# Performance work log

Measured on AMD Instinct MI355X. Metric: run time of the kernel, lower is better.

## Reference

```python
import jax, jax.numpy as jnp
import numpy as np

VOCAB, X_SIZE, H_SIZE, N_CLASSES = 50000, 300, 150, 5
DEPTH = 18                      # complete binary tree, N = 2^(DEPTH+1)-1 nodes
N_NODES = 2 ** (DEPTH + 1) - 1  # 524287
SCALE = 0.05                    # param init scale for numerical sanity


def setup_inputs() -> dict:
    key = jax.random.key(0)
    ks = jax.random.split(key, 8)
    return {
        "x_id": jax.random.randint(ks[0], (N_NODES,), 0, VOCAB, dtype=jnp.int32),
        "emb": jax.random.normal(ks[1], (VOCAB, X_SIZE), jnp.float32) * SCALE,
        "W_iou": jax.random.normal(ks[2], (X_SIZE, 3 * H_SIZE), jnp.float32) * SCALE,
        "U_iou": jax.random.normal(ks[3], (H_SIZE, 3 * H_SIZE), jnp.float32) * SCALE,
        "b_iou": jnp.zeros((3 * H_SIZE,), jnp.float32),
        "W_f": jax.random.normal(ks[4], (X_SIZE, H_SIZE), jnp.float32) * SCALE,
        "U_f": jax.random.normal(ks[5], (H_SIZE, H_SIZE), jnp.float32) * SCALE,
        "b_f": jnp.zeros((H_SIZE,), jnp.float32),
        "W_out": jax.random.normal(ks[6], (H_SIZE, N_CLASSES), jnp.float32) * SCALE,
        "b_out": jnp.zeros((N_CLASSES,), jnp.float32),
    }


def reference(x_id, emb, W_iou, U_iou, b_iou, W_f, U_f, b_f, W_out, b_out):
    # Child-Sum TreeLSTM propagated leaves->root over a complete binary tree
    # stored in heap layout: children of node i are 2i+1, 2i+2.
    N = x_id.shape[0]
    H = U_iou.shape[0]
    depth = int(np.log2(N + 1)) - 1

    x = emb[x_id]  # input_module: embedding lookup  [N, X]
    h = jnp.zeros((N, H), x.dtype)
    c = jnp.zeros((N, H), x.dtype)

    # level-batched topological propagation (19 static levels)
    for lvl in range(depth, -1, -1):
        s, e = 2 ** lvl - 1, 2 ** (lvl + 1) - 1  # node range of this level
        xl = x[s:e]                              # [n_l, X]
        if lvl == depth:  # leaves: zero child state
            h_sum = jnp.zeros((e - s, H), x.dtype)
            fc_sum = jnp.zeros((e - s, H), x.dtype)
        else:
            # children of consecutive nodes are contiguous: [2s+1, 2e+1)
            hc = h[2 * s + 1:2 * e + 1].reshape(e - s, 2, H)
            cc = c[2 * s + 1:2 * e + 1].reshape(e - s, 2, H)
            h_sum = hc.sum(axis=1)               # reduce: sum child h
            # per-child forget gate
            f = jax.nn.sigmoid((xl @ W_f)[:, None, :] + hc @ U_f + b_f)
            fc_sum = (f * cc).sum(axis=1)
        iou = xl @ W_iou + h_sum @ U_iou + b_iou  # [n_l, 3H]
        i, o, u = jnp.split(iou, 3, axis=-1)
        c_new = jax.nn.sigmoid(i) * jnp.tanh(u) + fc_sum
        h_new = jax.nn.sigmoid(o) * jnp.tanh(c_new)
        h = h.at[s:e].set(h_new)
        c = c.at[s:e].set(c_new)

    return h @ W_out + b_out  # output_module: Linear(H, C)  [N, C]
```

## Files before the change

### kernel.cpp

```cpp
#include <hip/hip_runtime.h>
#include <cstdint>

typedef _Float16 f16_t;
typedef __attribute__((ext_vector_type(8))) _Float16 f16x8;
typedef __attribute__((ext_vector_type(4))) _Float16 f16x4;
typedef __attribute__((ext_vector_type(4))) float f32x4;

#define HP      160
#define NCOL    640
#define KXP     320
#define NNODES  524287
#define LEAF_S  262143
#define LEAF_M  262144
#define NVOCAB  50000
#define AST     168

__device__ __forceinline__ float frcp(float x) { return __builtin_amdgcn_rcpf(x); }
__device__ __forceinline__ float sigf(float x) { return frcp(1.0f + __expf(-x)); }
__device__ __forceinline__ float tanhf_(float x) {
  return 1.0f - 2.0f * frcp(1.0f + __expf(2.0f * x));
}
__device__ __forceinline__ f16x8 zero8() {
  f16x8 z;
#pragma unroll
  for (int i = 0; i < 8; ++i) z[i] = (_Float16)0.0f;
  return z;
}
__device__ __forceinline__ f32x4 zero4() {
  f32x4 z;
#pragma unroll
  for (int i = 0; i < 4; ++i) z[i] = 0.0f;
  return z;
}

__global__ void prep_params(const float* __restrict__ W_iou, const float* __restrict__ U_iou,
                            const float* __restrict__ b_iou, const float* __restrict__ W_f,
                            const float* __restrict__ U_f, const float* __restrict__ b_f,
                            f16_t* __restrict__ WreT, f16_t* __restrict__ UreT,
                            float* __restrict__ bre) {
  int idx = blockIdx.x * 256 + threadIdx.x;
  if (idx < NCOL * KXP) {
    int col = idx / KXP, k = idx % KXP;
    int j = col >> 2, g = col & 3;
    float v = 0.0f;
    if (k < 300 && j < 150) v = (g < 3) ? W_iou[k * 450 + g * 150 + j] : W_f[k * 150 + j];
    WreT[idx] = (f16_t)v;
  } else if (idx < NCOL * KXP + NCOL * HP) {
    int i2 = idx - NCOL * KXP;
    int col = i2 / HP, k = i2 % HP;
    int g = col / 160, j = col % 160;
    float v = 0.0f;
    if (k < 150 && j < 150) v = (g < 3) ? U_iou[k * 450 + g * 150 + j] : U_f[k * 150 + j];
    UreT[i2] = (f16_t)v;
  } else if (idx < NCOL * KXP + NCOL * HP + NCOL) {
    int col = idx - (NCOL * KXP + NCOL * HP);
    int j = col >> 2, g = col & 3;
    bre[col] = (j < 150) ? ((g < 3) ? b_iou[g * 150 + j] : b_f[j]) : 0.0f;
  }
}

__global__ __launch_bounds__(256) void gemm_p(const float* __restrict__ emb,
                                              const f16_t* __restrict__ WreT,
                                              const float* __restrict__ bre,
                                              f16_t* __restrict__ P) {
  __shared__ __align__(16) f16_t A_sh[64 * 328];
  __shared__ __align__(16) f16_t B_sh[128 * 40];
  const int tid = threadIdx.x;
  const int wid = tid >> 6, lane = tid & 63, l15 = lane & 15, q = lane >> 4;
  const int row0 = blockIdx.x * 64;

#pragma unroll
  for (int i = 0; i < 10; ++i) {
    int ch = tid + 256 * i;
    int r = ch / 40, kc = (ch % 40) * 8;
    int grow = row0 + r;
    f16x8 hv;
    if (grow < NVOCAB && kc + 8 <= 300) {
      float4 a = *(const float4*)&emb[grow * 300 + kc];
      float4 b = *(const float4*)&emb[grow * 300 + kc + 4];
      hv[0] = (_Float16)a.x; hv[1] = (_Float16)a.y; hv[2] = (_Float16)a.z; hv[3] = (_Float16)a.w;
      hv[4] = (_Float16)b.x; hv[5] = (_Float16)b.y; hv[6] = (_Float16)b.z; hv[7] = (_Float16)b.w;
    } else {
#pragma unroll
      for (int e = 0; e < 8; ++e) {
        int k = kc + e;
        float v = (grow < NVOCAB && k < 300) ? emb[grow * 300 + k] : 0.0f;
        hv[e] = (_Float16)v;
      }
    }
    *(f16x8*)&A_sh[r * 328 + kc] = hv;
  }
  __syncthreads();

  for (int bn = 0; bn < 5; ++bn) {
    const int col0 = bn * 128;
    f32x4 acc[8];
#pragma unroll
    for (int t = 0; t < 8; ++t) acc[t] = zero4();
    for (int kk = 0; kk < KXP; kk += 32) {
#pragma unroll
      for (int i = 0; i < 2; ++i) {
        int ch = tid + 256 * i;
        int cidx = ch >> 2, kc = (ch & 3) * 8;
        *(f16x8*)&B_sh[cidx * 40 + kc] =
            *(const f16x8*)&WreT[(col0 + cidx) * KXP + kk + kc];
      }
      __syncthreads();
      f16x8 af = *(const f16x8*)&A_sh[(16 * wid + l15) * 328 + kk + q * 8];
#pragma unroll
      for (int t = 0; t < 8; ++t) {
        f16x8 bfr = *(const f16x8*)&B_sh[(t * 16 + l15) * 40 + q * 8];
        acc[t] = __builtin_amdgcn_mfma_f32_16x16x32_f16(af, bfr, acc[t], 0, 0, 0);
      }
      __syncthreads();
    }
#pragma unroll
    for (int t = 0; t < 8; ++t) {
      int col = col0 + t * 16 + l15;
      float bias = bre[col];
#pragma unroll
      for (int r2 = 0; r2 < 4; ++r2) {
        int row = row0 + 16 * wid + q * 4 + r2;
        if (row < NVOCAB) P[(long)row * NCOL + col] = (f16_t)(acc[t][r2] + bias);
      }
    }
  }
}

__global__ void leafhc_kernel(const f16_t* __restrict__ P, f16_t* __restrict__ Hleaf,
                              f16_t* __restrict__ Cleaf) {
  int idx = blockIdx.x * 256 + threadIdx.x;
  if (idx >= NVOCAB * 80) return;
  int v = idx / 80, t = idx % 80;
  f16x8 pk = *(const f16x8*)&P[(long)v * NCOL + t * 8];
#pragma unroll
  for (int e = 0; e < 2; ++e) {
    float iv = (float)pk[e * 4 + 0], ov = (float)pk[e * 4 + 1], uv = (float)pk[e * 4 + 2];
    float cl = sigf(iv) * tanhf_(uv);
    float hl = sigf(ov) * tanhf_(cl);
    Hleaf[(long)v * HP + t * 2 + e] = (f16_t)hl;
    Cleaf[(long)v * HP + t * 2 + e] = (f16_t)cl;
  }
}

__global__ void oleaf_kernel(const f16_t* __restrict__ Hleaf, const float* __restrict__ W_out,
                             const float* __restrict__ b_out, float* __restrict__ Oleaf) {
  const int tid = threadIdx.x;
  const int row = blockIdx.x * 16 + (tid >> 4), l = tid & 15;
  if (row >= NVOCAB) return;
  float acc[5] = {0, 0, 0, 0, 0};
  for (int j = l; j < 150; j += 16) {
    float hv = (float)Hleaf[(long)row * HP + j];
#pragma unroll
    for (int m = 0; m < 5; ++m) acc[m] += hv * W_out[j * 5 + m];
  }
#pragma unroll
  for (int m = 0; m < 5; ++m) {
    float vv = acc[m];
    vv += __shfl_xor(vv, 1);
    vv += __shfl_xor(vv, 2);
    vv += __shfl_xor(vv, 4);
    vv += __shfl_xor(vv, 8);
    if (l == 0) Oleaf[(long)row * 8 + m] = vv + b_out[m];
  }
}

__global__ void leafout_kernel(const int* __restrict__ x_id, const float* __restrict__ Oleaf,
                               float* __restrict__ out) {
  int leaf = blockIdx.x * 256 + threadIdx.x;
  int xv = x_id[LEAF_S + leaf];
  const float* O = Oleaf + (long)xv * 8;
  float4 o4 = *(const float4*)O;
  float o5 = O[4];
  long base = ((long)LEAF_S + leaf) * 5;
  out[base + 0] = o4.x; out[base + 1] = o4.y; out[base + 2] = o4.z;
  out[base + 3] = o4.w; out[base + 4] = o5;
}

__global__ __launch_bounds__(256, 3) void level17_kernel(
    const int* __restrict__ x_id, const f16_t* __restrict__ P,
    const f16_t* __restrict__ UreT, const f16_t* __restrict__ Hleaf,
    const f16_t* __restrict__ Cleaf, f16_t* __restrict__ Hout,
    f16_t* __restrict__ Cout, const float* __restrict__ W_out,
    const float* __restrict__ b_out, float* __restrict__ out) {
  __shared__ __align__(16) f16_t A_sh[64 * AST];
  __shared__ __align__(16) f16_t B_sh[128 * 40];
  const int tid = threadIdx.x;
  const int wid = tid >> 6, lane = tid & 63, l15 = lane & 15, q = lane >> 4;
  const int p0 = blockIdx.x * 32;
  const int s1 = (1 << 17) - 1;
  const long childbase = 2L * s1 + 1 + 2 * p0;

#pragma unroll
  for (int i = 0; i < 5; ++i) {
    int ch = tid + 256 * i;
    int r = ch / 20, kc = (ch % 20) * 8;
    int xv = x_id[childbase + r];
    *(f16x8*)&A_sh[r * AST + kc] = *(const f16x8*)&Hleaf[(long)xv * HP + kc];
  }
  __syncthreads();

  int xvp[2], xvl[2], xvr[2];
#pragma unroll
  for (int rr = 0; rr < 2; ++rr) {
    int pl = 8 * wid + 2 * q + rr;
    xvp[rr] = x_id[(long)s1 + p0 + pl];
    xvl[rr] = x_id[childbase + 2 * pl];
    xvr[rr] = x_id[childbase + 2 * pl + 1];
  }
  float oacc[2][5] = {};

  for (int jt = 0; jt < 5; ++jt) {
    const int j0 = jt * 32;
    f32x4 acc[4][2];
#pragma unroll
    for (int g = 0; g < 4; ++g)
#pragma unroll
      for (int jh = 0; jh < 2; ++jh) acc[g][jh] = zero4();

    for (int kk = 0; kk < HP; kk += 32) {
#pragma unroll
      for (int i = 0; i < 2; ++i) {
        int ch = tid + 256 * i;
        int cidx = ch >> 2, kc = (ch & 3) * 8;
        int g = cidx >> 5, jj = cidx & 31;
        int col = g * HP + j0 + jj;
        *(f16x8*)&B_sh[cidx * 40 + kc] = *(const f16x8*)&UreT[col * HP + kk + kc];
      }
      __syncthreads();
      f16x8 af = *(const f16x8*)&A_sh[(16 * wid + l15) * AST + kk + q * 8];
#pragma unroll
      for (int g = 0; g < 4; ++g)
#pragma unroll
        for (int jh = 0; jh < 2; ++jh) {
          f16x8 bfr = *(const f16x8*)&B_sh[(g * 32 + jh * 16 + l15) * 40 + q * 8];
          acc[g][jh] = __builtin_amdgcn_mfma_f32_16x16x32_f16(af, bfr, acc[g][jh], 0, 0, 0);
        }
      __syncthreads();
    }

#pragma unroll
    for (int rr = 0; rr < 2; ++rr) {
      const int r = rr * 2;
      const int pl = 8 * wid + 2 * q + rr;
      const f16_t* Prp = P + (long)xvp[rr] * NCOL;
#pragma unroll
      for (int jh = 0; jh < 2; ++jh) {
        const int j = j0 + jh * 16 + l15;
        f16x4 pp = *(const f16x4*)&Prp[j * 4];
        float ipre = (float)pp[0] + acc[0][jh][r] + acc[0][jh][r + 1];
        float opre = (float)pp[1] + acc[1][jh][r] + acc[1][jh][r + 1];
        float upre = (float)pp[2] + acc[2][jh][r] + acc[2][jh][r + 1];
        float pf   = (float)pp[3];
        float fl = sigf(pf + acc[3][jh][r]);
        float fr = sigf(pf + acc[3][jh][r + 1]);
        float clv = (float)Cleaf[(long)xvl[rr] * HP + j];
        float crv = (float)Cleaf[(long)xvr[rr] * HP + j];
        float cn = sigf(ipre) * tanhf_(upre) + fl * clv + fr * crv;
        float hn = sigf(opre) * tanhf_(cn);
        Hout[(long)(p0 + pl) * HP + j] = (f16_t)hn;
        Cout[(long)(p0 + pl) * HP + j] = (f16_t)cn;
        int wbase = (j < 150) ? j * 5 : 0;
#pragma unroll
        for (int m = 0; m < 5; ++m) oacc[rr][m] += hn * W_out[wbase + m];
      }
    }
  }

#pragma unroll
  for (int rr = 0; rr < 2; ++rr) {
    int pl = 8 * wid + 2 * q + rr;
#pragma unroll
    for (int m = 0; m < 5; ++m) {
      float v = oacc[rr][m];
      v += __shfl_xor(v, 1);
      v += __shfl_xor(v, 2);
      v += __shfl_xor(v, 4);
      v += __shfl_xor(v, 8);
      if (l15 == 0) out[((long)s1 + p0 + pl) * 5 + m] = v + b_out[m];
    }
  }
}

template <bool LEAF>
__global__ __launch_bounds__(256, 3) void fused_kernel(
    const int* __restrict__ x_id, const f16_t* __restrict__ P,
    const f16_t* __restrict__ UreT, const f16_t* __restrict__ Hc,
    const f16_t* __restrict__ Cc, f16_t* __restrict__ Hout,
    f16_t* __restrict__ Cout, const float* __restrict__ W_out,
    const float* __restrict__ b_out, float* __restrict__ out, int s1, int M1) {
  __shared__ __align__(16) f16_t A_sh[64 * AST];
  __shared__ __align__(16) f16_t A2_sh[32 * AST];
  __shared__ __align__(16) f16_t B_sh[128 * 40];
  __shared__ f16_t C_sh[32 * 160];
  const int tid = threadIdx.x;
  const int wid = tid >> 6, lane = tid & 63, l15 = lane & 15, q = lane >> 4;
  const int p0 = blockIdx.x * 32;
  const long childbase = 2L * s1 + 1 + 2 * p0;

#pragma unroll
  for (int i = 0; i < 5; ++i) {
    int ch = tid + 256 * i;
    int r = ch / 20, kc = (ch % 20) * 8;
    f16x8 v;
    if (LEAF) {
      int xv = x_id[childbase + r];
      v = *(const f16x8*)&Hc[(long)xv * HP + kc];
    } else {
      v = *(const f16x8*)&Hc[(long)(2 * p0 + r) * HP + kc];
    }
    *(f16x8*)&A_sh[r * AST + kc] = v;
  }
  __syncthreads();

  int xvp[2], xvl[2], xvr[2];
#pragma unroll
  for (int rr = 0; rr < 2; ++rr) {
    int pl = 8 * wid + 2 * q + rr;
    long pn = (long)s1 + p0 + pl;
    xvp[rr] = x_id[pn];
    if (LEAF) {
      xvl[rr] = x_id[childbase + 2 * pl];
      xvr[rr] = x_id[childbase + 2 * pl + 1];
    }
  }
  float oacc1[2][5] = {};

  for (int jt = 0; jt < 5; ++jt) {
    const int j0 = jt * 32;
    f32x4 acc[4][2];
#pragma unroll
    for (int g = 0; g < 4; ++g)
#pragma unroll
      for (int jh = 0; jh < 2; ++jh) acc[g][jh] = zero4();

    for (int kk = 0; kk < HP; kk += 32) {
#pragma unroll
      for (int i = 0; i < 2; ++i) {
        int ch = tid + 256 * i;
        int cidx = ch >> 2, kc = (ch & 3) * 8;
        int g = cidx >> 5, jj = cidx & 31;
        int col = g * HP + j0 + jj;
        *(f16x8*)&B_sh[cidx * 40 + kc] = *(const f16x8*)&UreT[col * HP + kk + kc];
      }
      __syncthreads();
      f16x8 af = *(const f16x8*)&A_sh[(16 * wid + l15) * AST + kk + q * 8];
#pragma unroll
      for (int g = 0; g < 4; ++g)
#pragma unroll
        for (int jh = 0; jh < 2; ++jh) {
          f16x8 bfr = *(const f16x8*)&B_sh[(g * 32 + jh * 16 + l15) * 40 + q * 8];
          acc[g][jh] = __builtin_amdgcn_mfma_f32_16x16x32_f16(af, bfr, acc[g][jh], 0, 0, 0);
        }
      __syncthreads();
    }

#pragma unroll
    for (int rr = 0; rr < 2; ++rr) {
      const int r = rr * 2;
      const int lr0 = 16 * wid + q * 4 + r;
      const int pl = lr0 >> 1;
      const f16_t* Prp = P + (long)xvp[rr] * NCOL;
#pragma unroll
      for (int jh = 0; jh < 2; ++jh) {
        const int j = j0 + jh * 16 + l15;
        f16x4 pp = *(const f16x4*)&Prp[j * 4];
        float ipre = (float)pp[0] + acc[0][jh][r] + acc[0][jh][r + 1];
        float opre = (float)pp[1] + acc[1][jh][r] + acc[1][jh][r + 1];
        float upre = (float)pp[2] + acc[2][jh][r] + acc[2][jh][r + 1];
        float pf   = (float)pp[3];
        float fl = sigf(pf + acc[3][jh][r]);
        float fr = sigf(pf + acc[3][jh][r + 1]);
        float clv, crv;
        if (LEAF) {
          clv = (float)Cc[(long)xvl[rr] * HP + j];
          crv = (float)Cc[(long)xvr[rr] * HP + j];
        } else {
          clv = (float)Cc[(long)(2 * p0 + lr0) * HP + j];
          crv = (float)Cc[(long)(2 * p0 + lr0 + 1) * HP + j];
        }
        float cn = sigf(ipre) * tanhf_(upre) + fl * clv + fr * crv;
        float hn = sigf(opre) * tanhf_(cn);
        A2_sh[pl * AST + j] = (f16_t)hn;
        C_sh[pl * 160 + j] = (f16_t)cn;
        int wbase = (j < 150) ? j * 5 : 0;
#pragma unroll
        for (int m = 0; m < 5; ++m) oacc1[rr][m] += hn * W_out[wbase + m];
      }
    }
  }

#pragma unroll
  for (int rr = 0; rr < 2; ++rr) {
    int pl = 8 * wid + 2 * q + rr;
#pragma unroll
    for (int m = 0; m < 5; ++m) {
      float v = oacc1[rr][m];
      v += __shfl_xor(v, 1);
      v += __shfl_xor(v, 2);
      v += __shfl_xor(v, 4);
      v += __shfl_xor(v, 8);
      if (l15 == 0) out[((long)s1 + p0 + pl) * 5 + m] = v + b_out[m];
    }
  }

  const int s2 = (s1 - 1) >> 1;
  const int p02 = p0 >> 1;
  const bool act2 = (wid < 2);
  int xvp2[2];
#pragma unroll
  for (int rr = 0; rr < 2; ++rr) {
    int pl = 8 * wid + 2 * q + rr;
    long pn = (long)s2 + p02 + (act2 ? pl : 0);
    xvp2[rr] = x_id[pn];
  }
  float oacc2[2][5] = {};

  for (int jt = 0; jt < 5; ++jt) {
    const int j0 = jt * 32;
    f32x4 acc[4][2];
#pragma unroll
    for (int g = 0; g < 4; ++g)
#pragma unroll
      for (int jh = 0; jh < 2; ++jh) acc[g][jh] = zero4();

    for (int kk = 0; kk < HP; kk += 32) {
#pragma unroll
      for (int i = 0; i < 2; ++i) {
        int ch = tid + 256 * i;
        int cidx = ch >> 2, kc = (ch & 3) * 8;
        int g = cidx >> 5, jj = cidx & 31;
        int col = g * HP + j0 + jj;
        *(f16x8*)&B_sh[cidx * 40 + kc] = *(const f16x8*)&UreT[col * HP + kk + kc];
      }
      __syncthreads();
      if (act2) {
        f16x8 af = *(const f16x8*)&A2_sh[(16 * wid + l15) * AST + kk + q * 8];
#pragma unroll
        for (int g = 0; g < 4; ++g)
#pragma unroll
          for (int jh = 0; jh < 2; ++jh) {
            f16x8 bfr = *(const f16x8*)&B_sh[(g * 32 + jh * 16 + l15) * 40 + q * 8];
            acc[g][jh] = __builtin_amdgcn_mfma_f32_16x16x32_f16(af, bfr, acc[g][jh], 0, 0, 0);
          }
      }
      __syncthreads();
    }

    if (act2) {
#pragma unroll
      for (int rr = 0; rr < 2; ++rr) {
        const int r = rr * 2;
        const int lr0 = 16 * wid + q * 4 + r;
        const int pl = lr0 >> 1;
        const f16_t* Prp = P + (long)xvp2[rr] * NCOL;
#pragma unroll
        for (int jh = 0; jh < 2; ++jh) {
          const int j = j0 + jh * 16 + l15;
          f16x4 pp = *(const f16x4*)&Prp[j * 4];
          float ipre = (float)pp[0] + acc[0][jh][r] + acc[0][jh][r + 1];
          float opre = (float)pp[1] + acc[1][jh][r] + acc[1][jh][r + 1];
          float upre = (float)pp[2] + acc[2][jh][r] + acc[2][jh][r + 1];
          float pf   = (float)pp[3];
          float fl = sigf(pf + acc[3][jh][r]);
          float fr = sigf(pf + acc[3][jh][r + 1]);
          float clv = (float)C_sh[lr0 * 160 + j];
          float crv = (float)C_sh[(lr0 + 1) * 160 + j];
          float cn = sigf(ipre) * tanhf_(upre) + fl * clv + fr * crv;
          float hn = sigf(opre) * tanhf_(cn);
          Hout[(long)(p02 + pl) * HP + j] = (f16_t)hn;
          Cout[(long)(p02 + pl) * HP + j] = (f16_t)cn;
          int wbase = (j < 150) ? j * 5 : 0;
#pragma unroll
          for (int m = 0; m < 5; ++m) oacc2[rr][m] += hn * W_out[wbase + m];
        }
      }
    }
  }

  if (act2) {
#pragma unroll
    for (int rr = 0; rr < 2; ++rr) {
      int pl = 8 * wid + 2 * q + rr;
#pragma unroll
      for (int m = 0; m < 5; ++m) {
        float v = oacc2[rr][m];
        v += __shfl_xor(v, 1);
        v += __shfl_xor(v, 2);
        v += __shfl_xor(v, 4);
        v += __shfl_xor(v, 8);
        if (l15 == 0) out[((long)s2 + p02 + pl) * 5 + m] = v + b_out[m];
      }
    }
  }
}

__global__ __launch_bounds__(256) void small_level(
    const int* __restrict__ x_id, const f16_t* __restrict__ P,
    const f16_t* __restrict__ UreT, const f16_t* __restrict__ Hc,
    const f16_t* __restrict__ Cc, f16_t* __restrict__ Hp, f16_t* __restrict__ Cp,
    const float* __restrict__ W_out, const float* __restrict__ b_out,
    float* __restrict__ out, int s) {
  __shared__ __align__(16) f16_t hlr[320];
  __shared__ float partial[4][5];
  const int tid = threadIdx.x;
  const int p = blockIdx.x;
  const long cb = (long)(2 * p) * HP;

  if (tid < 40) *(f16x8*)&hlr[tid * 8] = *(const f16x8*)&Hc[cb + tid * 8];
  __syncthreads();

  const int j = tid;
  float ai = 0.f, ao = 0.f, au = 0.f, afl = 0.f, afr = 0.f;
  float hn = 0.f;
  float contrib[5] = {0.f, 0.f, 0.f, 0.f, 0.f};
  if (j < HP) {
    const f16_t* Ui = &UreT[(long)(0 * HP + j) * HP];
    const f16_t* Uo = &UreT[(long)(1 * HP + j) * HP];
    const f16_t* Uu = &UreT[(long)(2 * HP + j) * HP];
    const f16_t* Uf = &UreT[(long)(3 * HP + j) * HP];
#pragma unroll 5
    for (int k8 = 0; k8 < 19; ++k8) {
      f16x8 hl8 = *(const f16x8*)&hlr[k8 * 8];
      f16x8 hr8 = *(const f16x8*)&hlr[160 + k8 * 8];
      f16x8 ui8 = *(const f16x8*)&Ui[k8 * 8];
      f16x8 uo8 = *(const f16x8*)&Uo[k8 * 8];
      f16x8 uu8 = *(const f16x8*)&Uu[k8 * 8];
      f16x8 uf8 = *(const f16x8*)&Uf[k8 * 8];
#pragma unroll
      for (int e = 0; e < 8; ++e) {
        float hlv = (float)hl8[e], hrv = (float)hr8[e];
        float hsv = hlv + hrv;
        ai  += hsv * (float)ui8[e];
        ao  += hsv * (float)uo8[e];
        au  += hsv * (float)uu8[e];
        afl += hlv * (float)uf8[e];
        afr += hrv * (float)uf8[e];
      }
    }
    int xv = x_id[(long)s + p];
    f16x4 pp = *(const f16x4*)&P[(long)xv * NCOL + j * 4];
    float ipre = (float)pp[0] + ai;
    float opre = (float)pp[1] + ao;
    float upre = (float)pp[2] + au;
    float pf   = (float)pp[3];
    float fl = sigf(pf + afl), fr = sigf(pf + afr);
    float clv = (float)Cc[cb + j];
    float crv = (float)Cc[cb + HP + j];
    float cn = sigf(ipre) * tanhf_(upre) + fl * clv + fr * crv;
    hn = sigf(opre) * tanhf_(cn);
    Hp[(long)p * HP + j] = (f16_t)hn;
    Cp[(long)p * HP + j] = (f16_t)cn;
    int wbase = (j < 150) ? j * 5 : 0;
#pragma unroll
    for (int m = 0; m < 5; ++m) contrib[m] = hn * W_out[wbase + m];
  }
  const int w = tid >> 6, l = tid & 63;
#pragma unroll
  for (int m = 0; m < 5; ++m) {
    float v = contrib[m];
    v += __shfl_xor(v, 1);  v += __shfl_xor(v, 2);  v += __shfl_xor(v, 4);
    v += __shfl_xor(v, 8);  v += __shfl_xor(v, 16); v += __shfl_xor(v, 32);
    if (l == 0) partial[w][m] = v;
  }
  __syncthreads();
  if (tid < 5) {
    float v = partial[0][tid] + partial[1][tid] + partial[2][tid] + partial[3][tid];
    out[((long)s + p) * 5 + tid] = v + b_out[tid];
  }
}

extern "C" void kernel_launch(void* const* d_in, const int* in_sizes, int n_in,
                              void* d_out, int out_size, void* d_ws, size_t ws_size,
                              hipStream_t stream) {
  const int* x_id   = (const int*)d_in[0];
  const float* emb  = (const float*)d_in[1];
  const float* W_iou = (const float*)d_in[2];
  const float* U_iou = (const float*)d_in[3];
  const float* b_iou = (const float*)d_in[4];
  const float* W_f   = (const float*)d_in[5];
  const float* U_f   = (const float*)d_in[6];
  const float* b_f   = (const float*)d_in[7];
  const float* W_out = (const float*)d_in[8];
  const float* b_out = (const float*)d_in[9];
  float* out = (float*)d_out;
  char* ws = (char*)d_ws;

  f16_t* WreT  = (f16_t*)(ws + 0);
  f16_t* UreT  = (f16_t*)(ws + 409600);
  float* bre   = (float*)(ws + 614400);
  f16_t* P     = (f16_t*)(ws + 616960);
  f16_t* Hleaf = (f16_t*)(ws + 64616960);
  f16_t* Cleaf = (f16_t*)(ws + 80616960);
  float* Oleaf = (float*)(ws + 96616960);
  f16_t* H17   = (f16_t*)(ws + 96616960);
  f16_t* C17   = (f16_t*)(ws + 138560000);
  f16_t* H15 = (f16_t*)(ws + 64616960);
  f16_t* C15 = (f16_t*)(ws + 75102720);
  f16_t* H13 = (f16_t*)(ws + 96616960);
  f16_t* C13 = (f16_t*)(ws + 99238400);
  char* vb = ws + 85588480;
  f16_t* VH[13]; f16_t* VC[13];
  for (int L = 12; L >= 0; --L) {
    size_t rows = (size_t)1 << L;
    VH[L] = (f16_t*)vb; vb += rows * 320;
    VC[L] = (f16_t*)vb; vb += rows * 320;
  }

  prep_params<<<1203, 256, 0, stream>>>(W_iou, U_iou, b_iou, W_f, U_f, b_f, WreT, UreT, bre);
  gemm_p<<<782, 256, 0, stream>>>(emb, WreT, bre, P);
  leafhc_kernel<<<15625, 256, 0, stream>>>(P, Hleaf, Cleaf);
  oleaf_kernel<<<3125, 256, 0, stream>>>(Hleaf, W_out, b_out, Oleaf);
  leafout_kernel<<<1024, 256, 0, stream>>>(x_id, Oleaf, out);

  level17_kernel<<<4096, 256, 0, stream>>>(x_id, P, UreT, Hleaf, Cleaf, H17, C17,
                                           W_out, b_out, out);
  fused_kernel<false><<<2048, 256, 0, stream>>>(x_id, P, UreT, H17, C17, H15, C15,
                                                W_out, b_out, out, (1 << 16) - 1, 1 << 16);
  fused_kernel<false><<<512, 256, 0, stream>>>(x_id, P, UreT, H15, C15, H13, C13,
                                               W_out, b_out, out, (1 << 14) - 1, 1 << 14);
  small_level<<<4096, 256, 0, stream>>>(x_id, P, UreT, H13, C13, VH[12], VC[12],
                                        W_out, b_out, out, (1 << 12) - 1);
  for (int L = 11; L >= 0; --L) {
    small_level<<<(1 << L), 256, 0, stream>>>(x_id, P, UreT, VH[L + 1], VC[L + 1],
                                              VH[L], VC[L], W_out, b_out, out,
                                              (1 << L) - 1);
  }

  (void)in_sizes; (void)n_in; (void)out_size; (void)ws_size;
}
```

Baseline: 991.3 us.

## Batch four parents per block in small levels with interleaved U layout

The small_level kernel now processes four parent nodes per block, so each U weight load is reused across four parents instead of one. A new interleaved UP2 weight layout, built in prep_params, packs the i/o/u/f gates for two consecutive k values into one 8-wide f16 vector, giving coalesced loads across j. This cuts U-matrix traffic and block count for the upper levels, but raises register pressure, leaves blocks underfilled at the tiny top levels, and needs bounds guards on the child-row loads.

```diff
diff --git a/kernel.cpp b/kernel.cpp
--- a/kernel.cpp
+++ b/kernel.cpp
@@ -4,6 +4,7 @@
 typedef _Float16 f16_t;
 typedef __attribute__((ext_vector_type(8))) _Float16 f16x8;
 typedef __attribute__((ext_vector_type(4))) _Float16 f16x4;
+typedef __attribute__((ext_vector_type(2))) _Float16 f16x2;
 typedef __attribute__((ext_vector_type(4))) float f32x4;
 
 #define HP      160
@@ -14,6 +15,7 @@
 #define LEAF_M  262144
 #define NVOCAB  50000
 #define AST     168
+#define PPB     4
 
 __device__ __forceinline__ float frcp(float x) { return __builtin_amdgcn_rcpf(x); }
 __device__ __forceinline__ float sigf(float x) { return frcp(1.0f + __expf(-x)); }
@@ -37,7 +39,7 @@
                             const float* __restrict__ b_iou, const float* __restrict__ W_f,
                             const float* __restrict__ U_f, const float* __restrict__ b_f,
                             f16_t* __restrict__ WreT, f16_t* __restrict__ UreT,
-                            float* __restrict__ bre) {
+                            float* __restrict__ bre, f16_t* __restrict__ UP2) {
   int idx = blockIdx.x * 256 + threadIdx.x;
   if (idx < NCOL * KXP) {
     int col = idx / KXP, k = idx % KXP;
@@ -56,6 +58,14 @@
     int col = idx - (NCOL * KXP + NCOL * HP);
     int j = col >> 2, g = col & 3;
     bre[col] = (j < 150) ? ((g < 3) ? b_iou[g * 150 + j] : b_f[j]) : 0.0f;
+  } else if (idx < NCOL * KXP + NCOL * HP + NCOL + NCOL * HP) {
+    int i3 = idx - (NCOL * KXP + NCOL * HP + NCOL);
+    int slot = i3 & 7, t = i3 >> 3;
+    int j = t % 160, k2 = t / 160;
+    int k = 2 * k2 + (slot >> 2), g = slot & 3;
+    float v = 0.0f;
+    if (k < 150 && j < 150) v = (g < 3) ? U_iou[k * 450 + g * 150 + j] : U_f[k * 150 + j];
+    UP2[i3] = (f16_t)v;
   }
 }
 
@@ -497,76 +507,99 @@
 
 __global__ __launch_bounds__(256) void small_level(
     const int* __restrict__ x_id, const f16_t* __restrict__ P,
-    const f16_t* __restrict__ UreT, const f16_t* __restrict__ Hc,
+    const f16_t* __restrict__ UP2, const f16_t* __restrict__ Hc,
     const f16_t* __restrict__ Cc, f16_t* __restrict__ Hp, f16_t* __restrict__ Cp,
     const float* __restrict__ W_out, const float* __restrict__ b_out,
-    float* __restrict__ out, int s) {
-  __shared__ __align__(16) f16_t hlr[320];
-  __shared__ float partial[4][5];
+    float* __restrict__ out, int s, int M) {
+  __shared__ __align__(16) f16_t hlr[8 * 160];
+  __shared__ float partial[4][PPB][5];
   const int tid = threadIdx.x;
-  const int p = blockIdx.x;
-  const long cb = (long)(2 * p) * HP;
-
-  if (tid < 40) *(f16x8*)&hlr[tid * 8] = *(const f16x8*)&Hc[cb + tid * 8];
+  const int pbase = blockIdx.x * PPB;
+  const int crow0 = 2 * pbase;
+  const int rowsValid = 2 * M - crow0;
+
+  if (tid < 160) {
+    int r = tid / 20, kc = (tid % 20) * 8;
+    f16x8 v = (r < rowsValid) ? *(const f16x8*)&Hc[(long)(crow0 + r) * HP + kc] : zero8();
+    *(f16x8*)&hlr[r * 160 + kc] = v;
+  }
   __syncthreads();
 
   const int j = tid;
-  float ai = 0.f, ao = 0.f, au = 0.f, afl = 0.f, afr = 0.f;
-  float hn = 0.f;
-  float contrib[5] = {0.f, 0.f, 0.f, 0.f, 0.f};
+  float ai[PPB], ao[PPB], au[PPB], afl[PPB], afr[PPB];
+  float contrib[PPB][5];
+#pragma unroll
+  for (int pp = 0; pp < PPB; ++pp) {
+    ai[pp] = ao[pp] = au[pp] = afl[pp] = afr[pp] = 0.0f;
+#pragma unroll
+    for (int m = 0; m < 5; ++m) contrib[pp][m] = 0.0f;
+  }
+
   if (j < HP) {
-    const f16_t* Ui = &UreT[(long)(0 * HP + j) * HP];
-    const f16_t* Uo = &UreT[(long)(1 * HP + j) * HP];
-    const f16_t* Uu = &UreT[(long)(2 * HP + j) * HP];
-    const f16_t* Uf = &UreT[(long)(3 * HP + j) * HP];
+    const f16_t* Uj = UP2 + (long)j * 8;
 #pragma unroll 5
-    for (int k8 = 0; k8 < 19; ++k8) {
-      f16x8 hl8 = *(const f16x8*)&hlr[k8 * 8];
-      f16x8 hr8 = *(const f16x8*)&hlr[160 + k8 * 8];
-      f16x8 ui8 = *(const f16x8*)&Ui[k8 * 8];
-      f16x8 uo8 = *(const f16x8*)&Uo[k8 * 8];
-      f16x8 uu8 = *(const f16x8*)&Uu[k8 * 8];
-      f16x8 uf8 = *(const f16x8*)&Uf[k8 * 8];
-#pragma unroll
-      for (int e = 0; e < 8; ++e) {
-        float hlv = (float)hl8[e], hrv = (float)hr8[e];
-        float hsv = hlv + hrv;
-        ai  += hsv * (float)ui8[e];
-        ao  += hsv * (float)uo8[e];
-        au  += hsv * (float)uu8[e];
-        afl += hlv * (float)uf8[e];
-        afr += hrv * (float)uf8[e];
-      }
-    }
-    int xv = x_id[(long)s + p];
-    f16x4 pp = *(const f16x4*)&P[(long)xv * NCOL + j * 4];
-    float ipre = (float)pp[0] + ai;
-    float opre = (float)pp[1] + ao;
-    float upre = (float)pp[2] + au;
-    float pf   = (float)pp[3];
-    float fl = sigf(pf + afl), fr = sigf(pf + afr);
-    float clv = (float)Cc[cb + j];
-    float crv = (float)Cc[cb + HP + j];
-    float cn = sigf(ipre) * tanhf_(upre) + fl * clv + fr * crv;
-    hn = sigf(opre) * tanhf_(cn);
-    Hp[(long)p * HP + j] = (f16_t)hn;
-    Cp[(long)p * HP + j] = (f16_t)cn;
-    int wbase = (j < 150) ? j * 5 : 0;
-#pragma unroll
-    for (int m = 0; m < 5; ++m) contrib[m] = hn * W_out[wbase + m];
-  }
+    for (int k2 = 0; k2 < 75; ++k2) {
+      f16x8 u8 = *(const f16x8*)&Uj[(long)k2 * 1280];
+      float ui0 = (float)u8[0], uo0 = (float)u8[1], uu0 = (float)u8[2], uf0 = (float)u8[3];
+      float ui1 = (float)u8[4], uo1 = (float)u8[5], uu1 = (float)u8[6], uf1 = (float)u8[7];
+#pragma unroll
+      for (int pp = 0; pp < PPB; ++pp) {
+        f16x2 hl2 = *(const f16x2*)&hlr[(2 * pp) * 160 + 2 * k2];
+        f16x2 hr2 = *(const f16x2*)&hlr[(2 * pp + 1) * 160 + 2 * k2];
+        float hl0 = (float)hl2[0], hl1 = (float)hl2[1];
+        float hr0 = (float)hr2[0], hr1 = (float)hr2[1];
+        float hs0 = hl0 + hr0, hs1 = hl1 + hr1;
+        ai[pp]  += hs0 * ui0 + hs1 * ui1;
+        ao[pp]  += hs0 * uo0 + hs1 * uo1;
+        au[pp]  += hs0 * uu0 + hs1 * uu1;
+        afl[pp] += hl0 * uf0 + hl1 * uf1;
+        afr[pp] += hr0 * uf0 + hr1 * uf1;
+      }
+    }
+
+#pragma unroll
+    for (int pp = 0; pp < PPB; ++pp) {
+      int p = pbase + pp;
+      bool pv = (p < M);
+      int xv = x_id[(long)s + (pv ? p : 0)];
+      f16x4 ppx = *(const f16x4*)&P[(long)xv * NCOL + j * 4];
+      float ipre = (float)ppx[0] + ai[pp];
+      float opre = (float)ppx[1] + ao[pp];
+      float upre = (float)ppx[2] + au[pp];
+      float pf   = (float)ppx[3];
+      float fl = sigf(pf + afl[pp]), fr = sigf(pf + afr[pp]);
+      float clv = pv ? (float)Cc[(long)(crow0 + 2 * pp) * HP + j] : 0.0f;
+      float crv = pv ? (float)Cc[(long)(crow0 + 2 * pp + 1) * HP + j] : 0.0f;
+      float cn = sigf(ipre) * tanhf_(upre) + fl * clv + fr * crv;
+      float hn = sigf(opre) * tanhf_(cn);
+      if (pv) {
+        Hp[(long)p * HP + j] = (f16_t)hn;
+        Cp[(long)p * HP + j] = (f16_t)cn;
+      }
+      int wbase = (j < 150) ? j * 5 : 0;
+#pragma unroll
+      for (int m = 0; m < 5; ++m) contrib[pp][m] = hn * W_out[wbase + m];
+    }
+  }
+
   const int w = tid >> 6, l = tid & 63;
 #pragma unroll
-  for (int m = 0; m < 5; ++m) {
-    float v = contrib[m];
-    v += __shfl_xor(v, 1);  v += __shfl_xor(v, 2);  v += __shfl_xor(v, 4);
-    v += __shfl_xor(v, 8);  v += __shfl_xor(v, 16); v += __shfl_xor(v, 32);
-    if (l == 0) partial[w][m] = v;
-  }
+  for (int pp = 0; pp < PPB; ++pp)
+#pragma unroll
+    for (int m = 0; m < 5; ++m) {
+      float v = contrib[pp][m];
+      v += __shfl_xor(v, 1);  v += __shfl_xor(v, 2);  v += __shfl_xor(v, 4);
+      v += __shfl_xor(v, 8);  v += __shfl_xor(v, 16); v += __shfl_xor(v, 32);
+      if (l == 0) partial[w][pp][m] = v;
+    }
   __syncthreads();
-  if (tid < 5) {
-    float v = partial[0][tid] + partial[1][tid] + partial[2][tid] + partial[3][tid];
-    out[((long)s + p) * 5 + tid] = v + b_out[tid];
+  if (tid < PPB * 5) {
+    int pp = tid / 5, m = tid % 5;
+    int p = pbase + pp;
+    if (p < M) {
+      float v = partial[0][pp][m] + partial[1][pp][m] + partial[2][pp][m] + partial[3][pp][m];
+      out[((long)s + p) * 5 + m] = v + b_out[m];
+    }
   }
 }
 
@@ -599,6 +632,7 @@
   f16_t* C15 = (f16_t*)(ws + 75102720);
   f16_t* H13 = (f16_t*)(ws + 96616960);
   f16_t* C13 = (f16_t*)(ws + 99238400);
+  f16_t* UP2 = (f16_t*)(ws + 180503040);
   char* vb = ws + 85588480;
   f16_t* VH[13]; f16_t* VC[13];
   for (int L = 12; L >= 0; --L) {
@@ -607,7 +641,8 @@
     VC[L] = (f16_t*)vb; vb += rows * 320;
   }
 
-  prep_params<<<1203, 256, 0, stream>>>(W_iou, U_iou, b_iou, W_f, U_f, b_f, WreT, UreT, bre);
+  prep_params<<<1603, 256, 0, stream>>>(W_iou, U_iou, b_iou, W_f, U_f, b_f,
+                                        WreT, UreT, bre, UP2);
   gemm_p<<<782, 256, 0, stream>>>(emb, WreT, bre, P);
   leafhc_kernel<<<15625, 256, 0, stream>>>(P, Hleaf, Cleaf);
   oleaf_kernel<<<3125, 256, 0, stream>>>(Hleaf, W_out, b_out, Oleaf);
@@ -619,12 +654,14 @@
                                                 W_out, b_out, out, (1 << 16) - 1, 1 << 16);
   fused_kernel<false><<<512, 256, 0, stream>>>(x_id, P, UreT, H15, C15, H13, C13,
                                                W_out, b_out, out, (1 << 14) - 1, 1 << 14);
-  small_level<<<4096, 256, 0, stream>>>(x_id, P, UreT, H13, C13, VH[12], VC[12],
-                                        W_out, b_out, out, (1 << 12) - 1);
+  small_level<<<1024, 256, 0, stream>>>(x_id, P, UP2, H13, C13, VH[12], VC[12],
+                                        W_out, b_out, out, (1 << 12) - 1, 1 << 12);
   for (int L = 11; L >= 0; --L) {
-    small_level<<<(1 << L), 256, 0, stream>>>(x_id, P, UreT, VH[L + 1], VC[L + 1],
-                                              VH[L], VC[L], W_out, b_out, out,
-                                              (1 << L) - 1);
+    int M = 1 << L;
+    int nb = (M + PPB - 1) / PPB;
+    small_level<<<nb, 256, 0, stream>>>(x_id, P, UP2, VH[L + 1], VC[L + 1],
+                                        VH[L], VC[L], W_out, b_out, out,
+                                        M - 1, M);
   }
 
   (void)in_sizes; (void)n_in; (void)out_size; (void)ws_size;
```

Result: faster. 950.1 us (-4.2%).
